# Optimization experiments

Hardware: AMD Instinct MI355X
Metric: run time of the kernel (lower is better)

## Reference

```python
import jax, jax.numpy as jnp
import numpy as np

H = 1024   # hidden_size
I = 2048   # intermediate_size
E = 16     # num_experts
K = 2      # num_experts_per_tok
B, T = 2, 2048


def setup_inputs() -> dict:
    key = jax.random.key(0)
    k1, k2, k3, k4 = jax.random.split(key, 4)
    x = jax.random.normal(k1, (B, T, H), dtype=jnp.float32)
    # torch nn.Linear weight layout: [out_features, in_features]
    Wg = jax.random.normal(k2, (E, H), dtype=jnp.float32) * 0.02   # gate
    W1 = jax.random.normal(k3, (E, I, H), dtype=jnp.float32) * 0.02  # fc1 per expert
    W2 = jax.random.normal(k4, (E, H, I), dtype=jnp.float32) * 0.02  # fc2 per expert
    return {"x": x, "Wg": Wg, "W1": W1, "W2": W2}


def reference(x, Wg, W1, W2):
    Bq, Tq, Hq = x.shape
    nt = Bq * Tq
    x_flat = x.reshape(nt, Hq)                       # [nt, H]
    gate_logits = x_flat @ Wg.T                      # [nt, E]
    gate_probs = jax.nn.softmax(gate_logits, axis=-1)
    topk_vals, topk_idx = jax.lax.top_k(gate_probs, K)  # [nt, K]
    # dense combine weights: zero for unselected (token, expert) pairs
    rows = jnp.arange(nt)[:, None]                   # [nt, 1]
    cw = jnp.zeros((nt, E), dtype=x.dtype).at[rows, topk_idx].add(topk_vals)
    # per-expert dense SiLU-MLP; combine weight of 0 makes unselected
    # contributions exactly zero, matching the original gather/scatter math.
    y_flat = jnp.zeros_like(x_flat)
    for e in range(E):
        h = jax.nn.silu(x_flat @ W1[e].T)            # [nt, I]
        o = h @ W2[e].T                              # [nt, H]
        y_flat = y_flat + cw[:, e:e + 1] * o
    return y_flat.reshape(Bq, Tq, Hq)
```

## Files before the change

### kernel.cpp

```cpp
#include <hip/hip_runtime.h>
#include <hip/hip_bf16.h>

#define H_DIM 1024
#define I_DIM 2048
#define NEXP  16
#define NTOK  4096
#define BM 128
#define BN 128
#define BK 32
#define MAXS 10240
#define MAXRB (MAXS/BM)
#define PAIRS (NTOK*2)
#define SORT_T 256
#define PPT (PAIRS/SORT_T)

typedef __attribute__((ext_vector_type(8))) short short8;
typedef __attribute__((ext_vector_type(4))) float f32x4;

#define OFF_TOKE 256
#define OFF_TOKW 33024
#define OFF_TOS  65792
#define OFF_WOS  106752
#define OFF_H    147712
#define OFF_XBF  42090752ULL
#define OFF_WBF  50479360ULL
#define NEED_FULL 117588224ULL

#define GLDS16(gsrc, ldst) \
  __builtin_amdgcn_global_load_lds((const __attribute__((address_space(1))) void*)(gsrc), \
                                   (__attribute__((address_space(3))) void*)(ldst), 16, 0, 0)

__device__ inline short f2bf(float f) {
    union { float f; unsigned u; } v; v.f = f;
    unsigned u = v.u + 0x7FFFu + ((v.u >> 16) & 1u);
    return (short)(u >> 16);
}

__device__ inline short8 pack8(const float4 a, const float4 b) {
    return (short8){ f2bf(a.x), f2bf(a.y), f2bf(a.z), f2bf(a.w),
                     f2bf(b.x), f2bf(b.y), f2bf(b.z), f2bf(b.w) };
}

__global__ __launch_bounds__(256) void conv_kernel(
    const float* __restrict__ src, short* __restrict__ dst, int n8)
{
    int i = blockIdx.x * blockDim.x + threadIdx.x;
    const int stride = gridDim.x * blockDim.x;
    for (; i < n8; i += stride) {
        const float4 f0 = ((const float4*)src)[2*i];
        const float4 f1 = ((const float4*)src)[2*i+1];
        ((short8*)dst)[i] = pack8(f0, f1);
    }
}

__global__ __launch_bounds__(256) void gate_kernel(
    const float* __restrict__ x, const float* __restrict__ Wg,
    int* __restrict__ tokE, float* __restrict__ tokW)
{
    const int wave = (blockIdx.x * blockDim.x + threadIdx.x) >> 6;
    const int lane = threadIdx.x & 63;
    if (wave >= NTOK) return;
    const float* xr = x + (size_t)wave * H_DIM;

    float acc[NEXP];
#pragma unroll
    for (int e = 0; e < NEXP; e++) acc[e] = 0.f;
    for (int j = lane; j < H_DIM; j += 64) {
        const float xv = xr[j];
#pragma unroll
        for (int e = 0; e < NEXP; e++) acc[e] = fmaf(xv, Wg[e * H_DIM + j], acc[e]);
    }
#pragma unroll
    for (int off = 32; off; off >>= 1) {
#pragma unroll
        for (int e = 0; e < NEXP; e++) acc[e] += __shfl_xor(acc[e], off, 64);
    }
    if (lane == 0) {
        float m = acc[0];
#pragma unroll
        for (int e = 1; e < NEXP; e++) m = fmaxf(m, acc[e]);
        float p[NEXP]; float s = 0.f;
#pragma unroll
        for (int e = 0; e < NEXP; e++) { p[e] = __expf(acc[e] - m); s += p[e]; }
        int i1 = 0;
#pragma unroll
        for (int e = 1; e < NEXP; e++) if (acc[e] > acc[i1]) i1 = e;
        int i2 = -1;
#pragma unroll
        for (int e = 0; e < NEXP; e++) {
            if (e == i1) continue;
            if (i2 < 0 || acc[e] > acc[i2]) i2 = e;
        }
        const float inv = 1.f / s;
        tokE[wave*2+0] = i1; tokW[wave*2+0] = p[i1] * inv;
        tokE[wave*2+1] = i2; tokW[wave*2+1] = p[i2] * inv;
    }
}

__global__ __launch_bounds__(SORT_T) void sort_kernel(
    const int* __restrict__ tokE, const float* __restrict__ tokW,
    int* __restrict__ aoff, int* __restrict__ tok_of_slot, float* __restrict__ w_of_slot)
{
    __shared__ int hist[NEXP * SORT_T];
    __shared__ int tot[NEXP];
    __shared__ int aoff_l[NEXP + 1];

    const int tid = threadIdx.x;
    const int lane = tid & 63, wv = tid >> 6;

    int eloc[PPT];
#pragma unroll
    for (int i = 0; i < PPT; i++) eloc[i] = tokE[tid * PPT + i];

#pragma unroll
    for (int e = 0; e < NEXP; e++) hist[e * SORT_T + tid] = 0;
    __syncthreads();
#pragma unroll
    for (int i = 0; i < PPT; i++) hist[eloc[i] * SORT_T + tid]++;
    __syncthreads();

#pragma unroll
    for (int r = 0; r < 4; r++) {
        const int e = wv * 4 + r;
        const int base = e * SORT_T + lane * 4;
        int v0 = hist[base+0], v1 = hist[base+1], v2 = hist[base+2], v3 = hist[base+3];
        const int s = v0 + v1 + v2 + v3;
        int incl = s;
#pragma unroll
        for (int off = 1; off < 64; off <<= 1) {
            const int t = __shfl_up(incl, off, 64);
            if (lane >= off) incl += t;
        }
        int run = incl - s;
        hist[base+0] = run; run += v0;
        hist[base+1] = run; run += v1;
        hist[base+2] = run; run += v2;
        hist[base+3] = run;
        if (lane == 63) tot[e] = incl;
    }
    __syncthreads();

    if (tid == 0) {
        int acc = 0;
#pragma unroll
        for (int e = 0; e < NEXP; e++) {
            aoff_l[e] = acc; aoff[e] = acc;
            acc += ((tot[e] + BM - 1) / BM) * BM;
        }
        aoff_l[NEXP] = acc; aoff[NEXP] = acc;
    }
    __syncthreads();

#pragma unroll
    for (int i = 0; i < PPT; i++) {
        const int p = tid * PPT + i;
        const int e = eloc[i];
        const int idx = hist[e * SORT_T + tid]++;
        const int slot = aoff_l[e] + idx;
        tok_of_slot[slot] = p >> 1;
        w_of_slot[slot] = tokW[p];
    }
}

template<int MODE>
__global__ __launch_bounds__(256) void fc1_kernel_t(
    const void* __restrict__ xsrc, const void* __restrict__ w1src,
    const int* __restrict__ aoff, const int* __restrict__ tok_of_slot,
    short* __restrict__ h)
{
    const int total = aoff[NEXP];
    const int row0 = blockIdx.y * BM;
    if (row0 >= total) return;
    int e = 0;
    while (aoff[e+1] <= row0) e++;
    const int col0 = blockIdx.x * BN;

    __shared__ short As[BM*BK];
    __shared__ short Bs[BN*BK];

    const int tid = threadIdx.x, wid = tid>>6, lane = tid&63;
    const int wr = wid>>1, wc = wid&1;

    const int srow = wid*32 + (lane>>2);
    const int skc  = (lane&3)*8;

    int t0 = tok_of_slot[row0 + srow];      if (t0 < 0) t0 = 0;
    int t1 = tok_of_slot[row0 + srow + 16]; if (t1 < 0) t1 = 0;

    const short *sa0=nullptr,*sa1=nullptr,*sb0=nullptr,*sb1=nullptr;
    const float *fa0=nullptr,*fa1=nullptr,*fb0=nullptr,*fb1=nullptr;
    if constexpr (MODE == 0) {
        const short* xb = (const short*)xsrc;
        const short* wb = (const short*)w1src + (size_t)e * I_DIM * H_DIM;
        sa0 = xb + (size_t)t0 * H_DIM + skc;
        sa1 = xb + (size_t)t1 * H_DIM + skc;
        sb0 = wb + (size_t)(col0 + srow)      * H_DIM + skc;
        sb1 = wb + (size_t)(col0 + srow + 16) * H_DIM + skc;
    } else {
        const float* xf = (const float*)xsrc;
        const float* wf = (const float*)w1src + (size_t)e * I_DIM * H_DIM;
        fa0 = xf + (size_t)t0 * H_DIM + skc;
        fa1 = xf + (size_t)t1 * H_DIM + skc;
        fb0 = wf + (size_t)(col0 + srow)      * H_DIM + skc;
        fb1 = wf + (size_t)(col0 + srow + 16) * H_DIM + skc;
    }
    short* la0 = &As[(wid*2+0)*512];
    short* la1 = &As[(wid*2+1)*512];
    short* lb0 = &Bs[(wid*2+0)*512];
    short* lb1 = &Bs[(wid*2+1)*512];

    const int frow = lane & 15, fko = (lane>>4)*8;

    f32x4 acc[4][4];
#pragma unroll
    for (int m=0;m<4;m++)
#pragma unroll
        for (int n=0;n<4;n++) acc[m][n] = (f32x4){0.f,0.f,0.f,0.f};

    for (int k0 = 0; k0 < H_DIM; k0 += BK) {
        if constexpr (MODE == 0) {
            GLDS16(sa0 + k0, la0);
            GLDS16(sa1 + k0, la1);
            GLDS16(sb0 + k0, lb0);
            GLDS16(sb1 + k0, lb1);
        } else {
            const float4 a00 = *(const float4*)(fa0 + k0), a01 = *(const float4*)(fa0 + k0 + 4);
            const float4 a10 = *(const float4*)(fa1 + k0), a11 = *(const float4*)(fa1 + k0 + 4);
            const float4 b00 = *(const float4*)(fb0 + k0), b01 = *(const float4*)(fb0 + k0 + 4);
            const float4 b10 = *(const float4*)(fb1 + k0), b11 = *(const float4*)(fb1 + k0 + 4);
            *(short8*)&As[srow*32 + skc]      = pack8(a00, a01);
            *(short8*)&As[(srow+16)*32 + skc] = pack8(a10, a11);
            *(short8*)&Bs[srow*32 + skc]      = pack8(b00, b01);
            *(short8*)&Bs[(srow+16)*32 + skc] = pack8(b10, b11);
        }
        __syncthreads();

        short8 af[4], bfr[4];
#pragma unroll
        for (int m=0;m<4;m++) af[m]  = *(const short8*)&As[(wr*64 + m*16 + frow)*32 + fko];
#pragma unroll
        for (int n=0;n<4;n++) bfr[n] = *(const short8*)&Bs[(wc*64 + n*16 + frow)*32 + fko];
#pragma unroll
        for (int m=0;m<4;m++)
#pragma unroll
            for (int n=0;n<4;n++)
                acc[m][n] = __builtin_amdgcn_mfma_f32_16x16x32_bf16(af[m], bfr[n], acc[m][n], 0, 0, 0);
        __syncthreads();
    }

    const int mr0 = row0 + wr*64 + (lane>>4)*4;
    const int nc0 = col0 + wc*64 + (lane&15);
#pragma unroll
    for (int m=0;m<4;m++)
#pragma unroll
        for (int n=0;n<4;n++)
#pragma unroll
            for (int r=0;r<4;r++) {
                const float v = acc[m][n][r];
                const float sv = v / (1.f + __expf(-v));
                h[(size_t)(mr0 + m*16 + r) * I_DIM + nc0 + n*16] = f2bf(sv);
            }
}

template<int MODE>
__global__ __launch_bounds__(256) void fc2_kernel_t(
    const short* __restrict__ h, const void* __restrict__ w2src,
    const int* __restrict__ aoff, const int* __restrict__ tok_of_slot,
    const float* __restrict__ w_of_slot, float* __restrict__ y)
{
    const int total = aoff[NEXP];
    const int row0 = blockIdx.y * BM;
    if (row0 >= total) return;
    int e = 0;
    while (aoff[e+1] <= row0) e++;
    const int col0 = blockIdx.x * BN;

    __shared__ short As[BM*BK];
    __shared__ short Bs[BN*BK];

    const int tid = threadIdx.x, wid = tid>>6, lane = tid&63;
    const int wr = wid>>1, wc = wid&1;

    const int srow = wid*32 + (lane>>2);
    const int skc  = (lane&3)*8;

    const short* sa0 = h + (size_t)(row0 + srow)      * I_DIM + skc;
    const short* sa1 = h + (size_t)(row0 + srow + 16) * I_DIM + skc;

    const short *sb0=nullptr,*sb1=nullptr;
    const float *fb0=nullptr,*fb1=nullptr;
    if constexpr (MODE == 0) {
        const short* wb = (const short*)w2src + (size_t)e * H_DIM * I_DIM;
        sb0 = wb + (size_t)(col0 + srow)      * I_DIM + skc;
        sb1 = wb + (size_t)(col0 + srow + 16) * I_DIM + skc;
    } else {
        const float* wf = (const float*)w2src + (size_t)e * H_DIM * I_DIM;
        fb0 = wf + (size_t)(col0 + srow)      * I_DIM + skc;
        fb1 = wf + (size_t)(col0 + srow + 16) * I_DIM + skc;
    }
    short* la0 = &As[(wid*2+0)*512];
    short* la1 = &As[(wid*2+1)*512];
    short* lb0 = &Bs[(wid*2+0)*512];
    short* lb1 = &Bs[(wid*2+1)*512];

    const int frow = lane & 15, fko = (lane>>4)*8;

    f32x4 acc[4][4];
#pragma unroll
    for (int m=0;m<4;m++)
#pragma unroll
        for (int n=0;n<4;n++) acc[m][n] = (f32x4){0.f,0.f,0.f,0.f};

    for (int k0 = 0; k0 < I_DIM; k0 += BK) {
        GLDS16(sa0 + k0, la0);
        GLDS16(sa1 + k0, la1);
        if constexpr (MODE == 0) {
            GLDS16(sb0 + k0, lb0);
            GLDS16(sb1 + k0, lb1);
        } else {
            const float4 b00 = *(const float4*)(fb0 + k0), b01 = *(const float4*)(fb0 + k0 + 4);
            const float4 b10 = *(const float4*)(fb1 + k0), b11 = *(const float4*)(fb1 + k0 + 4);
            *(short8*)&Bs[srow*32 + skc]      = pack8(b00, b01);
            *(short8*)&Bs[(srow+16)*32 + skc] = pack8(b10, b11);
        }
        __syncthreads();

        short8 af[4], bfr[4];
#pragma unroll
        for (int m=0;m<4;m++) af[m]  = *(const short8*)&As[(wr*64 + m*16 + frow)*32 + fko];
#pragma unroll
        for (int n=0;n<4;n++) bfr[n] = *(const short8*)&Bs[(wc*64 + n*16 + frow)*32 + fko];
#pragma unroll
        for (int m=0;m<4;m++)
#pragma unroll
            for (int n=0;n<4;n++)
                acc[m][n] = __builtin_amdgcn_mfma_f32_16x16x32_bf16(af[m], bfr[n], acc[m][n], 0, 0, 0);
        __syncthreads();
    }

    const int mr0 = row0 + wr*64 + (lane>>4)*4;
    const int nc0 = col0 + wc*64 + (lane&15);
#pragma unroll
    for (int m=0;m<4;m++)
#pragma unroll
        for (int r=0;r<4;r++) {
            const int slot = mr0 + m*16 + r;
            const int tok = tok_of_slot[slot];
            if (tok < 0) continue;
            const float w = w_of_slot[slot];
#pragma unroll
            for (int n=0;n<4;n++)
                atomicAdd(&y[(size_t)tok * H_DIM + nc0 + n*16], w * acc[m][n][r]);
        }
}

extern "C" void kernel_launch(void* const* d_in, const int* in_sizes, int n_in,
                              void* d_out, int out_size, void* d_ws, size_t ws_size,
                              hipStream_t stream) {
    const float* x  = (const float*)d_in[0];
    const float* Wg = (const float*)d_in[1];
    const float* W1 = (const float*)d_in[2];
    const float* W2 = (const float*)d_in[3];
    float* y = (float*)d_out;

    char* ws = (char*)d_ws;
    int*   aoff        = (int*)  (ws + 128);
    int*   tokE        = (int*)  (ws + OFF_TOKE);
    float* tokW        = (float*)(ws + OFF_TOKW);
    int*   tok_of_slot = (int*)  (ws + OFF_TOS);
    float* w_of_slot   = (float*)(ws + OFF_WOS);
    short* h           = (short*)(ws + OFF_H);
    short* xbf         = (short*)(ws + OFF_XBF);
    short* wbf         = (short*)(ws + OFF_WBF);

    const bool full = (ws_size >= NEED_FULL);

    hipMemsetAsync(tok_of_slot, 0xFF, MAXS*4, stream);
    hipMemsetAsync(y, 0, (size_t)out_size * 4, stream);

    gate_kernel<<<NTOK/4, 256, 0, stream>>>(x, Wg, tokE, tokW);
    sort_kernel<<<1, SORT_T, 0, stream>>>(tokE, tokW, aoff, tok_of_slot, w_of_slot);

    if (full) {
        conv_kernel<<<2048, 256, 0, stream>>>(W1, wbf, NEXP*I_DIM*H_DIM/8);
        conv_kernel<<<2048, 256, 0, stream>>>(x, xbf, NTOK*H_DIM/8);
        fc1_kernel_t<0><<<dim3(I_DIM/BN, MAXRB), 256, 0, stream>>>(xbf, wbf, aoff, tok_of_slot, h);
        conv_kernel<<<2048, 256, 0, stream>>>(W2, wbf, NEXP*H_DIM*I_DIM/8);
        fc2_kernel_t<0><<<dim3(H_DIM/BN, MAXRB), 256, 0, stream>>>(h, wbf, aoff, tok_of_slot, w_of_slot, y);
    } else {
        fc1_kernel_t<1><<<dim3(I_DIM/BN, MAXRB), 256, 0, stream>>>(x, W1, aoff, tok_of_slot, h);
        fc2_kernel_t<1><<<dim3(H_DIM/BN, MAXRB), 256, 0, stream>>>(h, W2, aoff, tok_of_slot, w_of_slot, y);
    }
}
```

Before: 265.5 us.

## Fuse weight conversion with gating and FC1, add split-K to FC2

Merges the W1 and x bf16 conversions with the gate computation into one launch, and runs the W2 conversion alongside the FC1 GEMM blocks in a second launch so independent work can overlap. FC2 now splits K across two block groups, which doubles its grid and relies on the existing atomicAdd epilogue to combine partials. The gate loop is vectorised to float4 loads, and the workspace layout gains separate W1 and W2 bf16 buffers, with a fallback tier when workspace is smaller. The risks are more atomic traffic in FC2, a larger workspace requirement, and load imbalance between the mixed block types.

```diff
diff --git a/kernel.cpp b/kernel.cpp
--- a/kernel.cpp
+++ b/kernel.cpp
@@ -14,17 +14,25 @@
 #define SORT_T 256
 #define PPT (PAIRS/SORT_T)
 
+#define GATE_B (NTOK/4)
+#define C1_B   1024
+#define CX_B   128
+#define C2_B   512
+#define FC1_B  ((I_DIM/BN)*MAXRB)
+
 typedef __attribute__((ext_vector_type(8))) short short8;
 typedef __attribute__((ext_vector_type(4))) float f32x4;
 
 #define OFF_TOKE 256
-#define OFF_TOKW 33024
-#define OFF_TOS  65792
-#define OFF_WOS  106752
-#define OFF_H    147712
-#define OFF_XBF  42090752ULL
-#define OFF_WBF  50479360ULL
-#define NEED_FULL 117588224ULL
+#define OFF_TOKW (OFF_TOKE + PAIRS*4)
+#define OFF_TOS  (OFF_TOKW + PAIRS*4)
+#define OFF_WOS  (OFF_TOS + MAXS*4)
+#define OFF_H    (OFF_WOS + MAXS*4)
+#define OFF_XBF  (OFF_H + (size_t)MAXS*I_DIM*2)
+#define OFF_W1BF (OFF_XBF + (size_t)NTOK*H_DIM*2)
+#define OFF_W2BF (OFF_W1BF + (size_t)NEXP*I_DIM*H_DIM*2)
+#define NEED_B   OFF_W2BF
+#define NEED_A   (OFF_W2BF + (size_t)NEXP*I_DIM*H_DIM*2)
 
 #define GLDS16(gsrc, ldst) \
   __builtin_amdgcn_global_load_lds((const __attribute__((address_space(1))) void*)(gsrc), \
@@ -41,11 +49,11 @@
                      f2bf(b.x), f2bf(b.y), f2bf(b.z), f2bf(b.w) };
 }
 
-__global__ __launch_bounds__(256) void conv_kernel(
-    const float* __restrict__ src, short* __restrict__ dst, int n8)
-{
-    int i = blockIdx.x * blockDim.x + threadIdx.x;
-    const int stride = gridDim.x * blockDim.x;
+__device__ inline void conv_body(const float* __restrict__ src, short* __restrict__ dst,
+                                 int n8, int bid, int nb)
+{
+    int i = bid * 256 + threadIdx.x;
+    const int stride = nb * 256;
     for (; i < n8; i += stride) {
         const float4 f0 = ((const float4*)src)[2*i];
         const float4 f1 = ((const float4*)src)[2*i+1];
@@ -53,22 +61,24 @@
     }
 }
 
-__global__ __launch_bounds__(256) void gate_kernel(
-    const float* __restrict__ x, const float* __restrict__ Wg,
-    int* __restrict__ tokE, float* __restrict__ tokW)
-{
-    const int wave = (blockIdx.x * blockDim.x + threadIdx.x) >> 6;
+__device__ void gate_body(const float* __restrict__ x, const float* __restrict__ Wg,
+                          int* __restrict__ tokE, float* __restrict__ tokW, int blk)
+{
+    const int tok  = blk * 4 + (threadIdx.x >> 6);
     const int lane = threadIdx.x & 63;
-    if (wave >= NTOK) return;
-    const float* xr = x + (size_t)wave * H_DIM;
+    const float4* xr = (const float4*)(x + (size_t)tok * H_DIM);
 
     float acc[NEXP];
 #pragma unroll
     for (int e = 0; e < NEXP; e++) acc[e] = 0.f;
-    for (int j = lane; j < H_DIM; j += 64) {
-        const float xv = xr[j];
-#pragma unroll
-        for (int e = 0; e < NEXP; e++) acc[e] = fmaf(xv, Wg[e * H_DIM + j], acc[e]);
+#pragma unroll
+    for (int j = 0; j < H_DIM/4; j += 64) {
+        const float4 xv = xr[j + lane];
+#pragma unroll
+        for (int e = 0; e < NEXP; e++) {
+            const float4 wv = ((const float4*)(Wg + e * H_DIM))[j + lane];
+            acc[e] = fmaf(xv.x, wv.x, fmaf(xv.y, wv.y, fmaf(xv.z, wv.z, fmaf(xv.w, wv.w, acc[e]))));
+        }
     }
 #pragma unroll
     for (int off = 32; off; off >>= 1) {
@@ -92,88 +102,22 @@
             if (i2 < 0 || acc[e] > acc[i2]) i2 = e;
         }
         const float inv = 1.f / s;
-        tokE[wave*2+0] = i1; tokW[wave*2+0] = p[i1] * inv;
-        tokE[wave*2+1] = i2; tokW[wave*2+1] = p[i2] * inv;
-    }
-}
-
-__global__ __launch_bounds__(SORT_T) void sort_kernel(
-    const int* __restrict__ tokE, const float* __restrict__ tokW,
-    int* __restrict__ aoff, int* __restrict__ tok_of_slot, float* __restrict__ w_of_slot)
-{
-    __shared__ int hist[NEXP * SORT_T];
-    __shared__ int tot[NEXP];
-    __shared__ int aoff_l[NEXP + 1];
-
-    const int tid = threadIdx.x;
-    const int lane = tid & 63, wv = tid >> 6;
-
-    int eloc[PPT];
-#pragma unroll
-    for (int i = 0; i < PPT; i++) eloc[i] = tokE[tid * PPT + i];
-
-#pragma unroll
-    for (int e = 0; e < NEXP; e++) hist[e * SORT_T + tid] = 0;
-    __syncthreads();
-#pragma unroll
-    for (int i = 0; i < PPT; i++) hist[eloc[i] * SORT_T + tid]++;
-    __syncthreads();
-
-#pragma unroll
-    for (int r = 0; r < 4; r++) {
-        const int e = wv * 4 + r;
-        const int base = e * SORT_T + lane * 4;
-        int v0 = hist[base+0], v1 = hist[base+1], v2 = hist[base+2], v3 = hist[base+3];
-        const int s = v0 + v1 + v2 + v3;
-        int incl = s;
-#pragma unroll
-        for (int off = 1; off < 64; off <<= 1) {
-            const int t = __shfl_up(incl, off, 64);
-            if (lane >= off) incl += t;
-        }
-        int run = incl - s;
-        hist[base+0] = run; run += v0;
-        hist[base+1] = run; run += v1;
-        hist[base+2] = run; run += v2;
-        hist[base+3] = run;
-        if (lane == 63) tot[e] = incl;
-    }
-    __syncthreads();
-
-    if (tid == 0) {
-        int acc = 0;
-#pragma unroll
-        for (int e = 0; e < NEXP; e++) {
-            aoff_l[e] = acc; aoff[e] = acc;
-            acc += ((tot[e] + BM - 1) / BM) * BM;
-        }
-        aoff_l[NEXP] = acc; aoff[NEXP] = acc;
-    }
-    __syncthreads();
-
-#pragma unroll
-    for (int i = 0; i < PPT; i++) {
-        const int p = tid * PPT + i;
-        const int e = eloc[i];
-        const int idx = hist[e * SORT_T + tid]++;
-        const int slot = aoff_l[e] + idx;
-        tok_of_slot[slot] = p >> 1;
-        w_of_slot[slot] = tokW[p];
+        tokE[tok*2+0] = i1; tokW[tok*2+0] = p[i1] * inv;
+        tokE[tok*2+1] = i2; tokW[tok*2+1] = p[i2] * inv;
     }
 }
 
 template<int MODE>
-__global__ __launch_bounds__(256) void fc1_kernel_t(
-    const void* __restrict__ xsrc, const void* __restrict__ w1src,
-    const int* __restrict__ aoff, const int* __restrict__ tok_of_slot,
-    short* __restrict__ h)
+__device__ void fc1_body(const void* __restrict__ xsrc, const void* __restrict__ w1src,
+                         const int* __restrict__ aoff, const int* __restrict__ tok_of_slot,
+                         short* __restrict__ h, int colb, int rowb)
 {
     const int total = aoff[NEXP];
-    const int row0 = blockIdx.y * BM;
+    const int row0 = rowb * BM;
     if (row0 >= total) return;
     int e = 0;
     while (aoff[e+1] <= row0) e++;
-    const int col0 = blockIdx.x * BN;
+    const int col0 = colb * BN;
 
     __shared__ short As[BM*BK];
     __shared__ short Bs[BN*BK];
@@ -263,17 +207,17 @@
 }
 
 template<int MODE>
-__global__ __launch_bounds__(256) void fc2_kernel_t(
-    const short* __restrict__ h, const void* __restrict__ w2src,
-    const int* __restrict__ aoff, const int* __restrict__ tok_of_slot,
-    const float* __restrict__ w_of_slot, float* __restrict__ y)
+__device__ void fc2_body(const short* __restrict__ h, const void* __restrict__ w2src,
+                         const int* __restrict__ aoff, const int* __restrict__ tok_of_slot,
+                         const float* __restrict__ w_of_slot, float* __restrict__ y,
+                         int colb, int rowb, int kbeg, int klen)
 {
     const int total = aoff[NEXP];
-    const int row0 = blockIdx.y * BM;
+    const int row0 = rowb * BM;
     if (row0 >= total) return;
     int e = 0;
     while (aoff[e+1] <= row0) e++;
-    const int col0 = blockIdx.x * BN;
+    const int col0 = colb * BN;
 
     __shared__ short As[BM*BK];
     __shared__ short Bs[BN*BK];
@@ -311,7 +255,7 @@
 #pragma unroll
         for (int n=0;n<4;n++) acc[m][n] = (f32x4){0.f,0.f,0.f,0.f};
 
-    for (int k0 = 0; k0 < I_DIM; k0 += BK) {
+    for (int k0 = kbeg; k0 < kbeg + klen; k0 += BK) {
         GLDS16(sa0 + k0, la0);
         GLDS16(sa1 + k0, la1);
         if constexpr (MODE == 0) {
@@ -354,6 +298,132 @@
         }
 }
 
+__global__ __launch_bounds__(256) void conv_kernel(
+    const float* __restrict__ src, short* __restrict__ dst, int n8)
+{
+    conv_body(src, dst, n8, blockIdx.x, gridDim.x);
+}
+
+__global__ __launch_bounds__(256) void mega1_kernel(
+    const float* __restrict__ x, const float* __restrict__ Wg, const float* __restrict__ W1,
+    int* __restrict__ tokE, float* __restrict__ tokW,
+    short* __restrict__ w1bf, short* __restrict__ xbf)
+{
+    int b = blockIdx.x;
+    if (b < C1_B) { conv_body(W1, w1bf, NEXP*I_DIM*H_DIM/8, b, C1_B); return; }
+    b -= C1_B;
+    if (b < CX_B) { conv_body(x, xbf, NTOK*H_DIM/8, b, CX_B); return; }
+    gate_body(x, Wg, tokE, tokW, b - CX_B);
+}
+
+__global__ __launch_bounds__(256) void gate_kernel(
+    const float* __restrict__ x, const float* __restrict__ Wg,
+    int* __restrict__ tokE, float* __restrict__ tokW)
+{
+    gate_body(x, Wg, tokE, tokW, blockIdx.x);
+}
+
+__global__ __launch_bounds__(SORT_T) void sort_kernel(
+    const int* __restrict__ tokE, const float* __restrict__ tokW,
+    int* __restrict__ aoff, int* __restrict__ tok_of_slot, float* __restrict__ w_of_slot)
+{
+    __shared__ int hist[NEXP * SORT_T];
+    __shared__ int tot[NEXP];
+    __shared__ int aoff_l[NEXP + 1];
+
+    const int tid = threadIdx.x;
+    const int lane = tid & 63, wv = tid >> 6;
+
+    int eloc[PPT];
+#pragma unroll
+    for (int i = 0; i < PPT; i++) eloc[i] = tokE[tid * PPT + i];
+
+#pragma unroll
+    for (int e = 0; e < NEXP; e++) hist[e * SORT_T + tid] = 0;
+    __syncthreads();
+#pragma unroll
+    for (int i = 0; i < PPT; i++) hist[eloc[i] * SORT_T + tid]++;
+    __syncthreads();
+
+#pragma unroll
+    for (int r = 0; r < 4; r++) {
+        const int e = wv * 4 + r;
+        const int base = e * SORT_T + lane * 4;
+        int v0 = hist[base+0], v1 = hist[base+1], v2 = hist[base+2], v3 = hist[base+3];
+        const int s = v0 + v1 + v2 + v3;
+        int incl = s;
+#pragma unroll
+        for (int off = 1; off < 64; off <<= 1) {
+            const int t = __shfl_up(incl, off, 64);
+            if (lane >= off) incl += t;
+        }
+        int run = incl - s;
+        hist[base+0] = run; run += v0;
+        hist[base+1] = run; run += v1;
+        hist[base+2] = run; run += v2;
+        hist[base+3] = run;
+        if (lane == 63) tot[e] = incl;
+    }
+    __syncthreads();
+
+    if (tid == 0) {
+        int acc = 0;
+#pragma unroll
+        for (int e = 0; e < NEXP; e++) {
+            aoff_l[e] = acc; aoff[e] = acc;
+            acc += ((tot[e] + BM - 1) / BM) * BM;
+        }
+        aoff_l[NEXP] = acc; aoff[NEXP] = acc;
+    }
+    __syncthreads();
+
+#pragma unroll
+    for (int i = 0; i < PPT; i++) {
+        const int p = tid * PPT + i;
+        const int e = eloc[i];
+        const int idx = hist[e * SORT_T + tid]++;
+        const int slot = aoff_l[e] + idx;
+        tok_of_slot[slot] = p >> 1;
+        w_of_slot[slot] = tokW[p];
+    }
+}
+
+template<bool CONV>
+__global__ __launch_bounds__(256) void mega2_kernel(
+    const float* __restrict__ W2, short* __restrict__ w2bf,
+    const void* __restrict__ xsrc, const void* __restrict__ w1src,
+    const int* __restrict__ aoff, const int* __restrict__ tok_of_slot,
+    short* __restrict__ h)
+{
+    int b = blockIdx.x;
+    if constexpr (CONV) {
+        if (b < C2_B) { conv_body(W2, w2bf, NEXP*H_DIM*I_DIM/8, b, C2_B); return; }
+        b -= C2_B;
+    }
+    fc1_body<0>(xsrc, w1src, aoff, tok_of_slot, h, b % (I_DIM/BN), b / (I_DIM/BN));
+}
+
+template<int MODE>
+__global__ __launch_bounds__(256) void fc1_kernel_w(
+    const void* __restrict__ xsrc, const void* __restrict__ w1src,
+    const int* __restrict__ aoff, const int* __restrict__ tok_of_slot,
+    short* __restrict__ h)
+{
+    fc1_body<MODE>(xsrc, w1src, aoff, tok_of_slot, h, blockIdx.x, blockIdx.y);
+}
+
+template<int MODE, int KS>
+__global__ __launch_bounds__(256) void fc2_kernel_w(
+    const short* __restrict__ h, const void* __restrict__ w2src,
+    const int* __restrict__ aoff, const int* __restrict__ tok_of_slot,
+    const float* __restrict__ w_of_slot, float* __restrict__ y)
+{
+    const int ks   = blockIdx.x % KS;
+    const int colb = blockIdx.x / KS;
+    fc2_body<MODE>(h, w2src, aoff, tok_of_slot, w_of_slot, y,
+                   colb, blockIdx.y, ks * (I_DIM / KS), I_DIM / KS);
+}
+
 extern "C" void kernel_launch(void* const* d_in, const int* in_sizes, int n_in,
                               void* d_out, int out_size, void* d_ws, size_t ws_size,
                               hipStream_t stream) {
@@ -371,24 +441,36 @@
     float* w_of_slot   = (float*)(ws + OFF_WOS);
     short* h           = (short*)(ws + OFF_H);
     short* xbf         = (short*)(ws + OFF_XBF);
-    short* wbf         = (short*)(ws + OFF_WBF);
-
-    const bool full = (ws_size >= NEED_FULL);
+    short* w1bf        = (short*)(ws + OFF_W1BF);
+    short* w2bf        = (short*)(ws + OFF_W2BF);
+
+    const bool tierA = (ws_size >= NEED_A);
+    const bool tierB = (ws_size >= NEED_B);
 
     hipMemsetAsync(tok_of_slot, 0xFF, MAXS*4, stream);
     hipMemsetAsync(y, 0, (size_t)out_size * 4, stream);
 
-    gate_kernel<<<NTOK/4, 256, 0, stream>>>(x, Wg, tokE, tokW);
-    sort_kernel<<<1, SORT_T, 0, stream>>>(tokE, tokW, aoff, tok_of_slot, w_of_slot);
-
-    if (full) {
-        conv_kernel<<<2048, 256, 0, stream>>>(W1, wbf, NEXP*I_DIM*H_DIM/8);
-        conv_kernel<<<2048, 256, 0, stream>>>(x, xbf, NTOK*H_DIM/8);
-        fc1_kernel_t<0><<<dim3(I_DIM/BN, MAXRB), 256, 0, stream>>>(xbf, wbf, aoff, tok_of_slot, h);
-        conv_kernel<<<2048, 256, 0, stream>>>(W2, wbf, NEXP*H_DIM*I_DIM/8);
-        fc2_kernel_t<0><<<dim3(H_DIM/BN, MAXRB), 256, 0, stream>>>(h, wbf, aoff, tok_of_slot, w_of_slot, y);
+    if (tierB) {
+        mega1_kernel<<<C1_B + CX_B + GATE_B, 256, 0, stream>>>(x, Wg, W1, tokE, tokW, w1bf, xbf);
+        sort_kernel<<<1, SORT_T, 0, stream>>>(tokE, tokW, aoff, tok_of_slot, w_of_slot);
+        if (tierA) {
+            mega2_kernel<true><<<C2_B + FC1_B, 256, 0, stream>>>(
+                W2, w2bf, xbf, w1bf, aoff, tok_of_slot, h);
+            fc2_kernel_w<0,2><<<dim3((H_DIM/BN)*2, MAXRB), 256, 0, stream>>>(
+                h, w2bf, aoff, tok_of_slot, w_of_slot, y);
+        } else {
+            mega2_kernel<false><<<FC1_B, 256, 0, stream>>>(
+                W2, nullptr, xbf, w1bf, aoff, tok_of_slot, h);
+            conv_kernel<<<2048, 256, 0, stream>>>(W2, w1bf, NEXP*H_DIM*I_DIM/8);
+            fc2_kernel_w<0,2><<<dim3((H_DIM/BN)*2, MAXRB), 256, 0, stream>>>(
+                h, w1bf, aoff, tok_of_slot, w_of_slot, y);
+        }
     } else {
-        fc1_kernel_t<1><<<dim3(I_DIM/BN, MAXRB), 256, 0, stream>>>(x, W1, aoff, tok_of_slot, h);
-        fc2_kernel_t<1><<<dim3(H_DIM/BN, MAXRB), 256, 0, stream>>>(h, W2, aoff, tok_of_slot, w_of_slot, y);
-    }
-}
+        gate_kernel<<<GATE_B, 256, 0, stream>>>(x, Wg, tokE, tokW);
+        sort_kernel<<<1, SORT_T, 0, stream>>>(tokE, tokW, aoff, tok_of_slot, w_of_slot);
+        fc1_kernel_w<1><<<dim3(I_DIM/BN, MAXRB), 256, 0, stream>>>(
+            x, W1, aoff, tok_of_slot, h);
+        fc2_kernel_w<1,1><<<dim3(H_DIM/BN, MAXRB), 256, 0, stream>>>(
+            h, W2, aoff, tok_of_slot, w_of_slot, y);
+    }
+}
```

Measured after the change: 376.6 us. 1.42x slower.
